# Kernel tuning notes

Measured on AMD Instinct MI355X. Metric: run time of the kernel, lower is better.

The kernel has to match this reference:

```python
import jax, jax.numpy as jnp
import numpy as np

B, S, D, H = 2, 2048, 2048, 16
HD = D // H  # 128


def setup_inputs() -> dict:
    key = jax.random.key(0)
    ks = jax.random.split(key, 6)
    sc = 0.02
    return {
        "x": jax.random.normal(ks[0], (B, S, D), jnp.float32),
        "attention_mask": jnp.ones((B, S), jnp.int32),
        "w_qkv": jax.random.normal(ks[1], (D, 3 * D), jnp.float32) * sc,
        "b_qkv": jnp.zeros((3 * D,), jnp.float32),
        "w_o": jax.random.normal(ks[2], (D, D), jnp.float32) * sc,
        "b_o": jnp.zeros((D,), jnp.float32),
        "ln1_w": jnp.ones((D,), jnp.float32),
        "w1": jax.random.normal(ks[3], (D, 8 * D), jnp.float32) * sc,
        "b1": jnp.zeros((8 * D,), jnp.float32),
        "w2": jax.random.normal(ks[4], (4 * D, D), jnp.float32) * sc,
        "b2": jnp.zeros((D,), jnp.float32),
        "ln2_w": jnp.ones((D,), jnp.float32),
    }


def rmsnorm(x, w, eps=1e-6):
    rms = jnp.sqrt(jnp.mean(x * x, axis=-1, keepdims=True) + eps)
    return w * (x / rms)


def rope_tables(seq_len, dim, base=10000.0):
    inv_freq = 1.0 / (base ** (jnp.arange(0, dim, 2, dtype=jnp.float32) / dim))
    t = jnp.arange(seq_len, dtype=jnp.float32)
    freqs = t[:, None] * inv_freq[None, :]          # [S, dim/2]
    emb = jnp.concatenate([freqs, freqs], axis=-1)  # [S, dim]
    return jnp.cos(emb), jnp.sin(emb)


def apply_rope(x, cos, sin):
    # Faithful to source: rotate pairs, then out = rot*cos + roll(rot,1)*sin
    xr = x.reshape(*x.shape[:-1], -1, 2)
    x1, x2 = xr[..., 0], xr[..., 1]
    rot = jnp.stack([-x2, x1], axis=-1).reshape(x.shape)
    return rot * cos + jnp.roll(rot, shift=1, axis=-1) * sin


def transformer_layer(x, attention_mask, w_qkv, b_qkv, w_o, b_o, ln1_w, w1, b1, w2, b2, ln2_w):
    residual = x
    qkv = x @ w_qkv + b_qkv                         # [B,S,3D]
    q, k, v = jnp.split(qkv, 3, axis=-1)
    split = lambda t: t.reshape(B, S, H, HD).transpose(0, 2, 1, 3)  # [B,H,S,HD]
    q, k, v = split(q), split(k), split(v)

    cos, sin = rope_tables(S, HD)                   # [S,HD], broadcasts over B,H
    q = apply_rope(q, cos, sin)
    k = apply_rope(k, cos, sin)

    scores = jnp.einsum("bhqd,bhkd->bhqk", q, k) / jnp.sqrt(jnp.float32(HD))
    mask = (attention_mask == 1)[:, None, None, :]  # [B,1,1,S]
    scores = jnp.where(mask, scores, -jnp.inf)
    attn = jax.nn.softmax(scores, axis=-1)
    out = jnp.einsum("bhqk,bhkd->bhqd", attn, v)
    out = out.transpose(0, 2, 1, 3).reshape(B, S, D)
    out = out @ w_o + b_o

    x = rmsnorm(out + residual, ln1_w)
    residual = x
    h = x @ w1 + b1                                 # [B,S,8D]
    h, gate = jnp.split(h, 2, axis=-1)
    h = h * jax.nn.gelu(gate, approximate=False)
    h = h @ w2 + b2
    return rmsnorm(h + residual, ln2_w)


def reference(x, attention_mask, w_qkv, b_qkv, w_o, b_o, ln1_w, w1, b1, w2, b2, ln2_w):
    return transformer_layer(x, attention_mask, w_qkv, b_qkv, w_o, b_o, ln1_w, w1, b1, w2, b2, ln2_w)
```

## Files before the change

kernel.cpp:

```cpp
#include <hip/hip_runtime.h>
#include <cstdint>

typedef unsigned short u16;
typedef __attribute__((ext_vector_type(8))) short short8;
typedef __attribute__((ext_vector_type(8))) unsigned short ushortx8;
typedef __attribute__((ext_vector_type(4))) float floatx4;

#define DEV __device__ __forceinline__

DEV u16 f2bf(float f) {
  union { float f; uint32_t u; } x; x.f = f;
  uint32_t r = x.u + 0x7fffu + ((x.u >> 16) & 1u);
  return (u16)(r >> 16);
}
DEV float bf2f(u16 h) {
  union { float f; uint32_t u; } x; x.u = ((uint32_t)h) << 16;
  return x.f;
}
DEV float fast_gelu(float g) {
  float u = 0.7978845608f * (g + 0.044715f * g * g * g);
  float e = __expf(-2.0f * fabsf(u));
  float th = (1.0f - e) / (1.0f + e);
  th = (u < 0.0f) ? -th : th;
  return 0.5f * g * (1.0f + th);
}
DEV void gload_lds16(const void* g, void* lds) {
  __builtin_amdgcn_global_load_lds(
      (const __attribute__((address_space(1))) char*)(uintptr_t)g,
      (__attribute__((address_space(3))) char*)(uintptr_t)lds, 16, 0, 0);
}


__global__ __launch_bounds__(256) void k_cvt_bf16(const float* __restrict__ in,
                                                  u16* __restrict__ out, int n) {
  int i = (blockIdx.x * 256 + threadIdx.x) * 4;
  if (i + 3 < n) {
    float4 v = *(const float4*)(in + i);
    ushort4 o;
    o.x = f2bf(v.x); o.y = f2bf(v.y); o.z = f2bf(v.z); o.w = f2bf(v.w);
    *(ushort4*)(out + i) = o;
  }
}

__global__ __launch_bounds__(256) void k_transpose_cvt(const float* __restrict__ W,
                                                       u16* __restrict__ Wt, int R, int C) {
  __shared__ u16 t[32][33];
  int tx = threadIdx.x & 31, ty = threadIdx.x >> 5;
  int r0 = blockIdx.y * 32, c0 = blockIdx.x * 32;
#pragma unroll
  for (int i = ty; i < 32; i += 8)
    t[i][tx] = f2bf(W[(size_t)(r0 + i) * C + c0 + tx]);
  __syncthreads();
#pragma unroll
  for (int i = ty; i < 32; i += 8)
    Wt[(size_t)(c0 + i) * R + r0 + tx] = t[tx][i];
}

__global__ __launch_bounds__(256) void k_transpose_w1p(const float* __restrict__ W,
                                                       u16* __restrict__ Wt) {
  __shared__ u16 t[32][33];
  int tx = threadIdx.x & 31, ty = threadIdx.x >> 5;
  int r0 = blockIdx.y * 32;
  int c0 = blockIdx.x * 32;
  int eta = c0 + tx;
  int Bq = eta >> 8, i = eta & 255, wn = (i >> 6) & 3, r = i & 63, n = r >> 4, tt = r & 15;
  int src = Bq * 128 + wn * 32 + (n & 1) * 16 + tt + ((n >= 2) ? 8192 : 0);
#pragma unroll
  for (int k = ty; k < 32; k += 8)
    t[k][tx] = f2bf(W[(size_t)(r0 + k) * 16384 + src]);
  __syncthreads();
#pragma unroll
  for (int i2 = ty; i2 < 32; i2 += 8)
    Wt[(size_t)(c0 + i2) * 2048 + r0 + tx] = t[tx][i2];
}

__global__ __launch_bounds__(256) void k_rope_tab(float* __restrict__ ct, float* __restrict__ st) {
  int i = blockIdx.x * 256 + threadIdx.x;
  int s = i >> 6, j = i & 63;
  float invf = 1.0f / powf(10000.0f, (float)j * (1.0f / 64.0f));
  float ang = (float)s * invf;
  ct[i] = cosf(ang);
  st[i] = sinf(ang);
}

__global__ __launch_bounds__(256) void k_rope_split(const u16* __restrict__ qkv,
                                                    const float* __restrict__ ct,
                                                    const float* __restrict__ st,
                                                    u16* __restrict__ qr, u16* __restrict__ kr) {
  int bs = blockIdx.x;
  int b = bs >> 11, s = bs & 2047;
  __shared__ float q[2048], k[2048];
  const u16* row = qkv + (size_t)bs * 6144;
  for (int i = threadIdx.x * 4; i < 2048; i += 1024) {
    ushort4 qa = *(const ushort4*)(row + i);
    ushort4 ka = *(const ushort4*)(row + 2048 + i);
    q[i] = bf2f(qa.x); q[i + 1] = bf2f(qa.y); q[i + 2] = bf2f(qa.z); q[i + 3] = bf2f(qa.w);
    k[i] = bf2f(ka.x); k[i + 1] = bf2f(ka.y); k[i + 2] = bf2f(ka.z); k[i + 3] = bf2f(ka.w);
  }
  __syncthreads();
  int i0 = threadIdx.x * 8;
  int h = i0 >> 7, d0 = i0 & 127;
  const float* qh = q + (h << 7);
  const float* kh = k + (h << 7);
  ushortx8 qo, ko;
#pragma unroll
  for (int e = 0; e < 8; ++e) {
    int d = d0 + e;
    int dm1 = (d + 127) & 127;
    float c = ct[(s << 6) + (d & 63)];
    float sn = st[(s << 6) + (d & 63)];
    float rq  = (d & 1)   ? qh[d - 1]   : -qh[d + 1];
    float rq1 = (dm1 & 1) ? qh[dm1 - 1] : -qh[dm1 + 1];
    float rk  = (d & 1)   ? kh[d - 1]   : -kh[d + 1];
    float rk1 = (dm1 & 1) ? kh[dm1 - 1] : -kh[dm1 + 1];
    qo[e] = f2bf(rq * c + rq1 * sn);
    ko[e] = f2bf(rk * c + rk1 * sn);
  }
  size_t obase = (((size_t)b * 16 + h) * 2048 + s) * 128 + d0;
  *(ushortx8*)(qr + obase) = qo;
  *(ushortx8*)(kr + obase) = ko;
}

__global__ __launch_bounds__(256) void k_v_transpose(const u16* __restrict__ qkv,
                                                     u16* __restrict__ vt) {
  __shared__ u16 t[32][33];
  int tx = threadIdx.x & 31, ty = threadIdx.x >> 5;
  int s0 = blockIdx.x * 32;
  int dm0 = (blockIdx.y & 63) * 32;
  int b = blockIdx.y >> 6;
#pragma unroll
  for (int i = ty; i < 32; i += 8)
    t[i][tx] = qkv[((size_t)(b * 2048) + s0 + i) * 6144 + 4096 + dm0 + tx];
  __syncthreads();
#pragma unroll
  for (int i = ty; i < 32; i += 8)
    vt[((size_t)b * 2048 + dm0 + i) * 2048 + s0 + tx] = t[tx][i];
}

template <int EPI>
__global__ __launch_bounds__(512, 2) void k_gemm256(const u16* __restrict__ A,
                                                    const u16* __restrict__ Bt,
                                                    void* __restrict__ C,
                                                    const float* __restrict__ bias,
                                                    int M, int N, int K, int nsplit) {
  __shared__ __align__(16) u16 lds[4][2][8192];
  const int tid = threadIdx.x;
  const int w = tid >> 6, lane = tid & 63;
  const int l15 = lane & 15, l4 = lane >> 4;
  const int wm = w >> 2, wn = w & 3;
  const int nbn = N >> 8;
  const int nbm = M >> 8;

  int bm, bn, split = 0;
  if (nsplit == 1 && nbm == 16 && (nbn & 7) == 0) {
    const int xcd = blockIdx.x & 7, l = blockIdx.x >> 3;
    const int xr = xcd >> 1, xc = xcd & 1;
    const int stn = l >> 4, lbm = (l >> 2) & 3, lbn = l & 3;
    bm = xr * 4 + lbm;
    bn = xc * (nbn >> 1) + stn * 4 + lbn;
  } else {
    const int nwg = gridDim.x;
    const int q = nwg >> 3, r8 = nwg & 7;
    const int xcd = blockIdx.x & 7, loc = blockIdx.x >> 3;
    const int swz = (xcd < r8 ? xcd * (q + 1) : r8 * (q + 1) + (xcd - r8) * q) + loc;
    const int ntiles = nwg / nsplit;
    split = swz / ntiles;
    const int tix = swz % ntiles;
    bm = tix / nbn; bn = tix % nbn;
  }
  const int klen = K / nsplit;
  const int kofs = split * klen;

  const size_t abase = (size_t)bm * 256 * K + kofs;
  const size_t bbase = (size_t)bn * 256 * K + kofs;
  const int nt = klen >> 5;

  const int sr = tid >> 2;
  const int sc = (tid & 3) ^ ((sr >> 1) & 3);
  auto stage = [&](int kt, int li, int op) {
    const u16* src = op ? (Bt + bbase) : (A + abase);
    gload_lds16(src + (size_t)(li * 128 + sr) * K + kt * 32 + sc * 8,
                (void*)&lds[kt & 3][op][(li * 512 + w * 64) * 8]);
  };

  const int fro = l15 * 32 + (l4 ^ ((l15 >> 1) & 3)) * 8;

  floatx4 acc[8][4];
  floatx4 zero = {0.f, 0.f, 0.f, 0.f};
#pragma unroll
  for (int m = 0; m < 8; ++m)
#pragma unroll
    for (int n = 0; n < 4; ++n) acc[m][n] = zero;

  for (int kt = 0; kt < 3; ++kt)
    if (kt < nt) {
      stage(kt, 0, 0); stage(kt, 0, 1);
      stage(kt, 1, 0); stage(kt, 1, 1);
    }

  for (int t = 0; t < nt; ++t) {
    const int buf = t & 3;
    if (t < nt - 2)       asm volatile("s_waitcnt vmcnt(8)" ::: "memory");
    else if (t == nt - 2) asm volatile("s_waitcnt vmcnt(4)" ::: "memory");
    else                  asm volatile("s_waitcnt vmcnt(0)" ::: "memory");
    __builtin_amdgcn_sched_barrier(0);
    __builtin_amdgcn_s_barrier();
    const u16* Ab = &lds[buf][0][wm * 4096 + fro];
    const u16* Bb = &lds[buf][1][wn * 2048 + fro];
    short8 av[4], bv[4];
#pragma unroll
    for (int n = 0; n < 4; ++n) bv[n] = *(const short8*)(Bb + n * 512);
#pragma unroll
    for (int i = 0; i < 4; ++i) av[i] = *(const short8*)(Ab + i * 512);
    if (t + 3 < nt) { stage(t + 3, 0, 0); stage(t + 3, 0, 1); }
    __builtin_amdgcn_sched_barrier(0);
    __builtin_amdgcn_s_barrier();
    asm volatile("s_waitcnt lgkmcnt(0)" ::: "memory");
    __builtin_amdgcn_sched_barrier(0);
    __builtin_amdgcn_s_setprio(1);
#pragma unroll
    for (int i = 0; i < 4; ++i)
#pragma unroll
      for (int n = 0; n < 4; ++n)
        acc[i][n] = __builtin_amdgcn_mfma_f32_16x16x32_bf16(av[i], bv[n], acc[i][n], 0, 0, 0);
    __builtin_amdgcn_s_setprio(0);
#pragma unroll
    for (int i = 0; i < 4; ++i) av[i] = *(const short8*)(Ab + (4 + i) * 512);
    if (t + 3 < nt) { stage(t + 3, 1, 0); stage(t + 3, 1, 1); }
    __builtin_amdgcn_sched_barrier(0);
    __builtin_amdgcn_s_barrier();
    asm volatile("s_waitcnt lgkmcnt(0)" ::: "memory");
    __builtin_amdgcn_sched_barrier(0);
    __builtin_amdgcn_s_setprio(1);
#pragma unroll
    for (int i = 0; i < 4; ++i)
#pragma unroll
      for (int n = 0; n < 4; ++n)
        acc[4 + i][n] = __builtin_amdgcn_mfma_f32_16x16x32_bf16(av[i], bv[n], acc[4 + i][n], 0, 0, 0);
    __builtin_amdgcn_s_setprio(0);
  }

  const int row0 = bm * 256 + wm * 128, col0 = bn * 256 + wn * 64;
  if (EPI == 2) {
    float* P = (float*)C + (size_t)split * M * N;
#pragma unroll
    for (int n = 0; n < 4; ++n) {
      int col = col0 + n * 16 + l15;
#pragma unroll
      for (int m = 0; m < 8; ++m)
#pragma unroll
        for (int j = 0; j < 4; ++j) {
          int row = row0 + m * 16 + l4 * 4 + j;
          P[(size_t)row * N + col] = acc[m][n][j];
        }
    }
  } else if (EPI == 3) {
    __syncthreads();
    u16* ep = ((u16*)lds) + w * 4096;
    const int colA = bn * 128 + wn * 32;
#pragma unroll
    for (int n = 0; n < 2; ++n) {
      float ba = bias[colA + n * 16 + l15];
      float bg = bias[8192 + colA + n * 16 + l15];
#pragma unroll
      for (int m = 0; m < 8; ++m)
#pragma unroll
        for (int j = 0; j < 4; ++j) {
          float a = acc[m][n][j] + ba;
          float g = acc[m][n + 2][j] + bg;
          ep[(m * 16 + l4 * 4 + j) * 32 + n * 16 + l15] = f2bf(a * fast_gelu(g));
        }
    }
    const int rr = lane >> 2, cg = lane & 3;
    u16* Cg = (u16*)C;
    const int Nact = N >> 1;
#pragma unroll
    for (int pass = 0; pass < 8; ++pass) {
      short8 v = *(const short8*)&ep[(pass * 16 + rr) * 32 + cg * 8];
      size_t grow = row0 + pass * 16 + rr;
      *(short8*)&Cg[grow * Nact + colA + cg * 8] = v;
    }
  } else {
    __syncthreads();
    u16* ep = ((u16*)lds) + w * 8192;
#pragma unroll
    for (int n = 0; n < 4; ++n) {
      float bb = bias[col0 + n * 16 + l15];
#pragma unroll
      for (int m = 0; m < 8; ++m)
#pragma unroll
        for (int j = 0; j < 4; ++j)
          ep[(m * 16 + l4 * 4 + j) * 64 + n * 16 + l15] = f2bf(acc[m][n][j] + bb);
    }
    const int rr = lane >> 3, cg = lane & 7;
    u16* Cg = (u16*)C;
#pragma unroll
    for (int pass = 0; pass < 16; ++pass) {
      short8 v = *(const short8*)&ep[(pass * 8 + rr) * 64 + cg * 8];
      size_t grow = row0 + pass * 8 + rr;
      *(short8*)&Cg[grow * N + col0 + cg * 8] = v;
    }
  }
}

__global__ __launch_bounds__(512, 4) void k_attn(const u16* __restrict__ Qr,
                                                 const u16* __restrict__ Kr,
                                                 const u16* __restrict__ Vt,
                                                 const int* __restrict__ mask,
                                                 u16* __restrict__ O) {
  constexpr int S = 2048, HD = 128, H = 16;
  __shared__ __align__(16) u16 Ksh[64 * 128];
  __shared__ __align__(16) u16 Vsh[128 * 64];
  __shared__ __align__(16) u16 Psh[8][16 * 72];
  __shared__ float Msh[2048];

  const int bid = blockIdx.x;
  const int xcd = bid & 7, local = bid >> 3;
  const int bh = xcd * 4 + (local >> 4);
  const int qt = local & 15;
  const int b = bh >> 4, h = bh & 15;
  const int tid = threadIdx.x, wave = tid >> 6, lane = tid & 63;
  const int l15 = lane & 15, l4 = lane >> 4;
  const size_t bhs = (size_t)(b * H + h);
  const u16* Qb = Qr + bhs * S * HD;
  const u16* Kb = Kr + bhs * S * HD;
  const u16* Vb = Vt + bhs * HD * S;

  for (int i = tid; i < 2048; i += 512)
    Msh[i] = (mask[b * S + i] == 1) ? 0.0f : -1e30f;

  const int qrow = qt * 128 + wave * 16 + l15;
  short8 qf[4];
#pragma unroll
  for (int kk = 0; kk < 4; ++kk)
    qf[kk] = *(const short8*)&Qb[(size_t)qrow * HD + kk * 32 + l4 * 8];

  float m_run[4], l_run[4];
  floatx4 o_acc[8];
  floatx4 zero = {0.f, 0.f, 0.f, 0.f};
#pragma unroll
  for (int j = 0; j < 4; ++j) { m_run[j] = -1e30f; l_run[j] = 0.f; }
#pragma unroll
  for (int n = 0; n < 8; ++n) o_acc[n] = zero;

  for (int ktile = 0; ktile < S / 64; ++ktile) {
    __syncthreads();
#pragma unroll
    for (int it = 0; it < 2; ++it) {
      int gi = it * 512 + tid;
      {
        int row = gi >> 4, g = gi & 15;
        int gs = (g & 8) | ((g ^ row) & 7);
        gload_lds16(Kb + (size_t)(ktile * 64 + row) * HD + gs * 8,
                    (char*)&Ksh[it * 4096 + wave * 512]);
      }
      {
        int row = gi >> 3, g = gi & 7;
        int gs = (g ^ row) & 7;
        gload_lds16(Vb + (size_t)row * S + ktile * 64 + gs * 8,
                    (char*)&Vsh[it * 4096 + wave * 512]);
      }
    }
    __syncthreads();

    floatx4 s_acc[4];
#pragma unroll
    for (int nf = 0; nf < 4; ++nf) s_acc[nf] = zero;
#pragma unroll
    for (int kk = 0; kk < 4; ++kk) {
#pragma unroll
      for (int nf = 0; nf < 4; ++nf) {
        int key = nf * 16 + l15;
        int G = kk * 4 + l4;
        int lg = (G & 8) | ((G ^ key) & 7);
        short8 kv = *(const short8*)&Ksh[key * 128 + lg * 8];
        s_acc[nf] = __builtin_amdgcn_mfma_f32_16x16x32_bf16(qf[kk], kv, s_acc[nf], 0, 0, 0);
      }
    }

    const float scale = 0.08838834764831845f;
    float p[4][4];
#pragma unroll
    for (int nf = 0; nf < 4; ++nf) {
      float ma = Msh[ktile * 64 + nf * 16 + l15];
#pragma unroll
      for (int j = 0; j < 4; ++j) p[nf][j] = s_acc[nf][j] * scale + ma;
    }
#pragma unroll
    for (int j = 0; j < 4; ++j) {
      float mx = fmaxf(fmaxf(p[0][j], p[1][j]), fmaxf(p[2][j], p[3][j]));
      mx = fmaxf(mx, __shfl_xor(mx, 1));
      mx = fmaxf(mx, __shfl_xor(mx, 2));
      mx = fmaxf(mx, __shfl_xor(mx, 4));
      mx = fmaxf(mx, __shfl_xor(mx, 8));
      float mnew = fmaxf(m_run[j], mx);
      float corr = __expf(m_run[j] - mnew);
      float ps = 0.f;
#pragma unroll
      for (int nf = 0; nf < 4; ++nf) {
        p[nf][j] = __expf(p[nf][j] - mnew);
        ps += p[nf][j];
      }
      ps += __shfl_xor(ps, 1); ps += __shfl_xor(ps, 2);
      ps += __shfl_xor(ps, 4); ps += __shfl_xor(ps, 8);
      l_run[j] = l_run[j] * corr + ps;
      m_run[j] = mnew;
#pragma unroll
      for (int n = 0; n < 8; ++n) o_acc[n][j] *= corr;
    }

#pragma unroll
    for (int nf = 0; nf < 4; ++nf)
#pragma unroll
      for (int j = 0; j < 4; ++j)
        Psh[wave][(l4 * 4 + j) * 72 + nf * 16 + l15] = f2bf(p[nf][j]);

#pragma unroll
    for (int ks = 0; ks < 2; ++ks) {
      short8 pa = *(const short8*)&Psh[wave][l15 * 72 + ks * 32 + l4 * 8];
#pragma unroll
      for (int nf2 = 0; nf2 < 8; ++nf2) {
        int hd = nf2 * 16 + l15;
        int G = ks * 4 + l4;
        short8 vv = *(const short8*)&Vsh[hd * 64 + ((G ^ hd) & 7) * 8];
        o_acc[nf2] = __builtin_amdgcn_mfma_f32_16x16x32_bf16(pa, vv, o_acc[nf2], 0, 0, 0);
      }
    }
  }

#pragma unroll
  for (int j = 0; j < 4; ++j) {
    float inv = 1.0f / l_run[j];
    int srow = qt * 128 + wave * 16 + l4 * 4 + j;
    size_t orow = ((size_t)b * S + srow) * 2048 + h * 128;
#pragma unroll
    for (int nf2 = 0; nf2 < 8; ++nf2)
      O[orow + nf2 * 16 + l15] = f2bf(o_acc[nf2][j] * inv);
  }
}

template <int OUTMODE>
__global__ __launch_bounds__(256) void k_rms_fuse(const float* __restrict__ p0,
                                                  const float* __restrict__ p1,
                                                  const float* __restrict__ bias,
                                                  const float* __restrict__ resid,
                                                  const float* __restrict__ w,
                                                  u16* __restrict__ ob,
                                                  float* __restrict__ of) {
  int row = blockIdx.x;
  int t = threadIdx.x;
  size_t base = (size_t)row * 2048 + t * 8;
  float4 a0 = *(const float4*)(p0 + base);
  float4 a1 = *(const float4*)(p0 + base + 4);
  float4 b0 = *(const float4*)(p1 + base);
  float4 b1 = *(const float4*)(p1 + base + 4);
  float4 r0 = *(const float4*)(resid + base);
  float4 r1 = *(const float4*)(resid + base + 4);
  float4 c0 = *(const float4*)(bias + t * 8);
  float4 c1 = *(const float4*)(bias + t * 8 + 4);
  float v[8];
  v[0] = a0.x + b0.x + r0.x + c0.x; v[1] = a0.y + b0.y + r0.y + c0.y;
  v[2] = a0.z + b0.z + r0.z + c0.z; v[3] = a0.w + b0.w + r0.w + c0.w;
  v[4] = a1.x + b1.x + r1.x + c1.x; v[5] = a1.y + b1.y + r1.y + c1.y;
  v[6] = a1.z + b1.z + r1.z + c1.z; v[7] = a1.w + b1.w + r1.w + c1.w;
  float ss = 0.f;
#pragma unroll
  for (int e = 0; e < 8; ++e) ss += v[e] * v[e];
#pragma unroll
  for (int d = 1; d < 64; d <<= 1) ss += __shfl_xor(ss, d);
  __shared__ float sred[4];
  if ((t & 63) == 0) sred[t >> 6] = ss;
  __syncthreads();
  float tot = sred[0] + sred[1] + sred[2] + sred[3];
  float scale = rsqrtf(tot * (1.0f / 2048.0f) + 1e-6f);
  const float* wp = w + t * 8;
  float o[8];
#pragma unroll
  for (int e = 0; e < 8; ++e) o[e] = v[e] * wp[e] * scale;
  if (OUTMODE == 1) {
    ushort4 q0, q1;
    q0.x = f2bf(o[0]); q0.y = f2bf(o[1]); q0.z = f2bf(o[2]); q0.w = f2bf(o[3]);
    q1.x = f2bf(o[4]); q1.y = f2bf(o[5]); q1.z = f2bf(o[6]); q1.w = f2bf(o[7]);
    *(ushort4*)(ob + base) = q0;
    *(ushort4*)(ob + base + 4) = q1;
  }
  {
    float4 f0, f1;
    f0.x = o[0]; f0.y = o[1]; f0.z = o[2]; f0.w = o[3];
    f1.x = o[4]; f1.y = o[5]; f1.z = o[6]; f1.w = o[7];
    *(float4*)(of + base) = f0;
    *(float4*)(of + base + 4) = f1;
  }
}

extern "C" void kernel_launch(void* const* d_in, const int* in_sizes, int n_in,
                              void* d_out, int out_size, void* d_ws, size_t ws_size,
                              hipStream_t stream) {
  const float* x     = (const float*)d_in[0];
  const int*   amask = (const int*)d_in[1];
  const float* w_qkv = (const float*)d_in[2];
  const float* b_qkv = (const float*)d_in[3];
  const float* w_o   = (const float*)d_in[4];
  const float* b_o   = (const float*)d_in[5];
  const float* ln1_w = (const float*)d_in[6];
  const float* w1    = (const float*)d_in[7];
  const float* b1    = (const float*)d_in[8];
  const float* w2    = (const float*)d_in[9];
  const float* b2    = (const float*)d_in[10];
  const float* ln2_w = (const float*)d_in[11];
  float* out = (float*)d_out;

  char* ws = (char*)d_ws;
  u16*   xb    = (u16*)(ws + 0);
  u16*   wqkvT = (u16*)(ws + 16777216);
  u16*   woT   = (u16*)(ws + 41943040);
  u16*   w1Tp  = (u16*)(ws + 50331648);
  u16*   w2T   = (u16*)(ws + 117440512);
  float* ctab  = (float*)(ws + 150994944);
  float* stab  = (float*)(ws + 151519232);
  u16*   qkv   = (u16*)(ws + 152043520);
  u16*   qr    = (u16*)(ws + 202375168);
  u16*   kr    = (u16*)(ws + 219152384);
  u16*   vt    = (u16*)(ws + 235929600);
  u16*   aout  = (u16*)(ws + 252706816);
  u16*   x1b   = (u16*)(ws + 303038464);
  float* x1f   = (float*)(ws + 319815680);
  float* p01a  = (float*)(ws + 152043520);
  u16*   act   = (u16*)(ws + 152043520);
  float* p01b  = (float*)(ws + 219152384);

  k_cvt_bf16<<<8192, 256, 0, stream>>>(x, xb, 4096 * 2048);
  k_transpose_cvt<<<dim3(192, 64), 256, 0, stream>>>(w_qkv, wqkvT, 2048, 6144);
  k_transpose_cvt<<<dim3(64, 64), 256, 0, stream>>>(w_o, woT, 2048, 2048);
  k_transpose_w1p<<<dim3(512, 64), 256, 0, stream>>>(w1, w1Tp);
  k_transpose_cvt<<<dim3(64, 256), 256, 0, stream>>>(w2, w2T, 8192, 2048);
  k_rope_tab<<<512, 256, 0, stream>>>(ctab, stab);

  k_gemm256<0><<<16 * 24, 512, 0, stream>>>(xb, wqkvT, qkv, b_qkv, 4096, 6144, 2048, 1);
  k_rope_split<<<4096, 256, 0, stream>>>(qkv, ctab, stab, qr, kr);
  k_v_transpose<<<dim3(64, 128), 256, 0, stream>>>(qkv, vt);
  k_attn<<<512, 512, 0, stream>>>(qr, kr, vt, amask, aout);

  k_gemm256<2><<<16 * 8 * 2, 512, 0, stream>>>(aout, woT, p01a, nullptr, 4096, 2048, 2048, 2);
  k_rms_fuse<1><<<4096, 256, 0, stream>>>(p01a, p01a + (size_t)4096 * 2048, b_o, x, ln1_w, x1b, x1f);

  k_gemm256<3><<<16 * 64, 512, 0, stream>>>(x1b, w1Tp, act, b1, 4096, 16384, 2048, 1);

  k_gemm256<2><<<16 * 8 * 2, 512, 0, stream>>>(act, w2T, p01b, nullptr, 4096, 2048, 8192, 2);
  k_rms_fuse<2><<<4096, 256, 0, stream>>>(p01b, p01b + (size_t)4096 * 2048, b2, x1f, ln2_w, nullptr, out);
}
```

Baseline: 936.1 us.

## Merge weight transposes, trim GEMM barriers, add lazy softmax rescaling

Three weight transpose-convert launches are merged into one kernel that picks its matrix from the block index, which removes launch overhead and tail effects. In the GEMM main loop, one of the two per-iteration workgroup barriers is removed and the other is moved after the first MFMA batch, cutting synchronisation stalls at the risk of LDS read/write hazards across buffers. In flash attention, the online-softmax max/rescale step is skipped when every lane's new max is within 8 of the running max. This avoids the shuffles and o_acc rescaling, but lets exponentials grow up to e^8 before being renormalised.

```diff
diff --git a/kernel.cpp b/kernel.cpp
--- a/kernel.cpp
+++ b/kernel.cpp
@@ -42,11 +42,21 @@
   }
 }
 
-__global__ __launch_bounds__(256) void k_transpose_cvt(const float* __restrict__ W,
-                                                       u16* __restrict__ Wt, int R, int C) {
+__global__ __launch_bounds__(256) void k_transpose_all(const float* __restrict__ Wq,
+                                                       u16* __restrict__ WqT,
+                                                       const float* __restrict__ Wo,
+                                                       u16* __restrict__ WoT,
+                                                       const float* __restrict__ W2,
+                                                       u16* __restrict__ W2T) {
   __shared__ u16 t[32][33];
+  int id = blockIdx.x;
+  const float* W; u16* Wt; int R, C, tix;
+  if (id < 12288)      { W = Wq; Wt = WqT; R = 2048; C = 6144; tix = id; }
+  else if (id < 16384) { W = Wo; Wt = WoT; R = 2048; C = 2048; tix = id - 12288; }
+  else                 { W = W2; Wt = W2T; R = 8192; C = 2048; tix = id - 16384; }
+  int ntc = C >> 5;
+  int c0 = (tix % ntc) * 32, r0 = (tix / ntc) * 32;
   int tx = threadIdx.x & 31, ty = threadIdx.x >> 5;
-  int r0 = blockIdx.y * 32, c0 = blockIdx.x * 32;
 #pragma unroll
   for (int i = ty; i < 32; i += 8)
     t[i][tx] = f2bf(W[(size_t)(r0 + i) * C + c0 + tx]);
@@ -213,8 +223,6 @@
 #pragma unroll
     for (int i = 0; i < 4; ++i) av[i] = *(const short8*)(Ab + i * 512);
     if (t + 3 < nt) { stage(t + 3, 0, 0); stage(t + 3, 0, 1); }
-    __builtin_amdgcn_sched_barrier(0);
-    __builtin_amdgcn_s_barrier();
     asm volatile("s_waitcnt lgkmcnt(0)" ::: "memory");
     __builtin_amdgcn_sched_barrier(0);
     __builtin_amdgcn_s_setprio(1);
@@ -224,11 +232,10 @@
       for (int n = 0; n < 4; ++n)
         acc[i][n] = __builtin_amdgcn_mfma_f32_16x16x32_bf16(av[i], bv[n], acc[i][n], 0, 0, 0);
     __builtin_amdgcn_s_setprio(0);
+    __builtin_amdgcn_s_barrier();
 #pragma unroll
     for (int i = 0; i < 4; ++i) av[i] = *(const short8*)(Ab + (4 + i) * 512);
     if (t + 3 < nt) { stage(t + 3, 1, 0); stage(t + 3, 1, 1); }
-    __builtin_amdgcn_sched_barrier(0);
-    __builtin_amdgcn_s_barrier();
     asm volatile("s_waitcnt lgkmcnt(0)" ::: "memory");
     __builtin_amdgcn_sched_barrier(0);
     __builtin_amdgcn_s_setprio(1);
@@ -388,13 +395,22 @@
     }
 #pragma unroll
     for (int j = 0; j < 4; ++j) {
-      float mx = fmaxf(fmaxf(p[0][j], p[1][j]), fmaxf(p[2][j], p[3][j]));
-      mx = fmaxf(mx, __shfl_xor(mx, 1));
-      mx = fmaxf(mx, __shfl_xor(mx, 2));
-      mx = fmaxf(mx, __shfl_xor(mx, 4));
-      mx = fmaxf(mx, __shfl_xor(mx, 8));
-      float mnew = fmaxf(m_run[j], mx);
-      float corr = __expf(m_run[j] - mnew);
+      float pm = fmaxf(fmaxf(p[0][j], p[1][j]), fmaxf(p[2][j], p[3][j]));
+      bool ok = __all(pm - m_run[j] <= 8.0f);
+      float mnew = m_run[j];
+      if (!ok) {
+        float mx = pm;
+        mx = fmaxf(mx, __shfl_xor(mx, 1));
+        mx = fmaxf(mx, __shfl_xor(mx, 2));
+        mx = fmaxf(mx, __shfl_xor(mx, 4));
+        mx = fmaxf(mx, __shfl_xor(mx, 8));
+        mnew = fmaxf(m_run[j], mx);
+        float corr = __expf(m_run[j] - mnew);
+        l_run[j] *= corr;
+#pragma unroll
+        for (int n = 0; n < 8; ++n) o_acc[n][j] *= corr;
+        m_run[j] = mnew;
+      }
       float ps = 0.f;
 #pragma unroll
       for (int nf = 0; nf < 4; ++nf) {
@@ -403,10 +419,7 @@
       }
       ps += __shfl_xor(ps, 1); ps += __shfl_xor(ps, 2);
       ps += __shfl_xor(ps, 4); ps += __shfl_xor(ps, 8);
-      l_run[j] = l_run[j] * corr + ps;
-      m_run[j] = mnew;
-#pragma unroll
-      for (int n = 0; n < 8; ++n) o_acc[n][j] *= corr;
+      l_run[j] += ps;
     }
 
 #pragma unroll
@@ -530,10 +543,8 @@
   float* p01b  = (float*)(ws + 219152384);
 
   k_cvt_bf16<<<8192, 256, 0, stream>>>(x, xb, 4096 * 2048);
-  k_transpose_cvt<<<dim3(192, 64), 256, 0, stream>>>(w_qkv, wqkvT, 2048, 6144);
-  k_transpose_cvt<<<dim3(64, 64), 256, 0, stream>>>(w_o, woT, 2048, 2048);
+  k_transpose_all<<<32768, 256, 0, stream>>>(w_qkv, wqkvT, w_o, woT, w2, w2T);
   k_transpose_w1p<<<dim3(512, 64), 256, 0, stream>>>(w1, w1Tp);
-  k_transpose_cvt<<<dim3(64, 256), 256, 0, stream>>>(w2, w2T, 8192, 2048);
   k_rope_tab<<<512, 256, 0, stream>>>(ctab, stab);
 
   k_gemm256<0><<<16 * 24, 512, 0, stream>>>(xb, wqkvT, qkv, b_qkv, 4096, 6144, 2048, 1);
```

After: 1.199 ms. +28.1%, slower.
